# Optimization experiments

Hardware: AMD Instinct MI355X
Metric: run time of the kernel (lower is better)

Reference implementation:

```python
import jax, jax.numpy as jnp
import numpy as np

E = 1024   # embed_dim
H = 16     # num_heads
D = E // H # head_dim = 64
S = 8192   # cache length
LN_EPS = 1e-6  # flax LayerNorm default


def _ln(x, scale, bias):
    m = jnp.mean(x, axis=-1, keepdims=True)
    v = jnp.mean(jnp.square(x - m), axis=-1, keepdims=True)
    return (x - m) * jax.lax.rsqrt(v + LN_EPS) * scale + bias


def setup_inputs() -> dict:
    key = jax.random.key(0)
    ks = jax.random.split(key, 16)
    w = lambda k, shape: jax.random.normal(k, shape, jnp.float32) * 0.02
    return {
        "x": jax.random.normal(ks[0], (E,), jnp.float32),
        "cache": jax.random.normal(ks[1], (2, S, H, D), jnp.float32),
        "Wv": w(ks[2], (E, E)), "bv": jnp.zeros((E,), jnp.float32),
        "Wq": w(ks[3], (E, E)), "bq": jnp.zeros((E,), jnp.float32),
        "Wk": w(ks[4], (E, E)), "bk": jnp.zeros((E,), jnp.float32),
        "Wo": w(ks[5], (E, E)), "bo": jnp.zeros((E,), jnp.float32),
        "W1": w(ks[6], (E, E)), "b1": jnp.zeros((E,), jnp.float32),
        "W2": w(ks[7], (E, E)), "b2": jnp.zeros((E,), jnp.float32),
        "ln1_s": jnp.ones((E,), jnp.float32), "ln1_b": jnp.zeros((E,), jnp.float32),
        "ln2_s": jnp.ones((E,), jnp.float32), "ln2_b": jnp.zeros((E,), jnp.float32),
        "eval_flag": 1,
    }


def reference(x, cache, Wv, bv, Wq, bq, Wk, bk, Wo, bo,
              W1, b1, W2, b2, ln1_s, ln1_b, ln2_s, ln2_b, eval_flag):
    # --- attention with shifting KV cache ---
    v_i = (x @ Wv + bv).reshape(1, H, D)
    q_i = (x @ Wq + bq).reshape(H, D)
    k_i = (x @ Wk + bk).reshape(1, H, D)
    v = jnp.concatenate((cache[0, 1:], v_i), axis=0)  # [S, H, D]
    k = jnp.concatenate((cache[1, 1:], k_i), axis=0)  # [S, H, D]
    mask = jnp.any(v != 0, axis=(1, 2))               # [S]
    attn = jnp.einsum('hd,khd->hk', q_i, k) / jnp.sqrt(jnp.float32(D))
    attn = jnp.where(mask, attn, -jnp.inf)
    attn = jax.nn.softmax(attn, axis=-1)              # [H, S]
    values = jnp.einsum('hk,khd->hd', attn, v).reshape(E)
    out_i = values @ Wo + bo
    new_cache = jnp.stack([v, k])                     # [2, S, H, D]

    # --- residual + LN + FFN (dropout deterministic => identity) ---
    h = _ln(x + out_i, ln1_s, ln1_b)
    ff = jax.nn.relu(h @ W1 + b1) @ W2 + b2
    h = _ln(h + ff, ln2_s, ln2_b)
    return (h, new_cache)
```

## Files before the change

### kernel.cpp

```cpp
#include <hip/hip_runtime.h>
#include <hip/hip_bf16.h>

#define SLEN 8192
#define EDIM 1024
#define NB2  512

typedef float f4 __attribute__((ext_vector_type(4)));


__device__ inline float2 blockSum512_2(float2 v, float2* lds) {
#pragma unroll
    for (int off = 32; off; off >>= 1) {
        v.x += __shfl_xor(v.x, off);
        v.y += __shfl_xor(v.y, off);
    }
    int w = threadIdx.x >> 6, ln = threadIdx.x & 63;
    __syncthreads();
    if (ln == 0) lds[w] = v;
    __syncthreads();
    float2 s = {0.f, 0.f};
#pragma unroll
    for (int i = 0; i < 8; ++i) { s.x += lds[i].x; s.y += lds[i].y; }
    return s;
}

__device__ inline float2 blockSum1024_2(float2 v, float2* lds) {
#pragma unroll
    for (int off = 32; off; off >>= 1) {
        v.x += __shfl_xor(v.x, off);
        v.y += __shfl_xor(v.y, off);
    }
    int w = threadIdx.x >> 6, ln = threadIdx.x & 63;
    __syncthreads();
    if (ln == 0) lds[w] = v;
    __syncthreads();
    float2 s = {0.f, 0.f};
#pragma unroll
    for (int i = 0; i < 16; ++i) { s.x += lds[i].x; s.y += lds[i].y; }
    return s;
}

__global__ __launch_bounds__(256) void qkv_partial(
    const float* __restrict__ Wq, const float* __restrict__ Wk,
    const float* __restrict__ Wv, const float* __restrict__ x,
    float* __restrict__ part) {
    int cg_ = blockIdx.x;
    int m = cg_ >> 2;
    const float* W = (m == 0) ? Wq : ((m == 1) ? Wk : Wv);
    int col = (cg_ & 3) * 256 + threadIdx.x;
    int r0 = blockIdx.y * 64;
    float acc = 0.f;
#pragma unroll 16
    for (int r = 0; r < 64; ++r)
        acc = fmaf(x[r0 + r], W[(r0 + r) * EDIM + col], acc);
    part[((size_t)m * 16 + blockIdx.y) * EDIM + col] = acc;
}

__global__ __launch_bounds__(512) void attn_copy(
    const float* __restrict__ cache,
    const float* __restrict__ qkvp,
    const float* __restrict__ bq, const float* __restrict__ bk,
    const float* __restrict__ bv,
    float* __restrict__ nv, float* __restrict__ nk,
    float* __restrict__ flag, float* __restrict__ score) {
    __shared__ float qs_l[1024];
    __shared__ float aux[1024];
    int b = blockIdx.x, tid = threadIdx.x;
    int w = tid >> 6, ld = tid & 63;
    int c = b >> 1;
    bool isK = (b & 1) != 0;
    int s0 = c * 16 + w * 2;

    if (isK) {
#pragma unroll
        for (int j = 0; j < 2; ++j) {
            int i = tid + 512 * j;
            float v = bq[i];
#pragma unroll
            for (int sl = 0; sl < 16; ++sl) v += qkvp[sl * EDIM + i];
            qs_l[i] = v * 0.125f;
        }
        if (b == 1023) {
#pragma unroll
            for (int j = 0; j < 2; ++j) {
                int i = tid + 512 * j;
                float v = bk[i];
#pragma unroll
                for (int sl = 0; sl < 16; ++sl) v += qkvp[(16 + sl) * EDIM + i];
                aux[i] = v;
            }
        }
    } else if (b == 1022) {
#pragma unroll
        for (int j = 0; j < 2; ++j) {
            int i = tid + 512 * j;
            float v = bv[i];
#pragma unroll
            for (int sl = 0; sl < 16; ++sl) v += qkvp[(32 + sl) * EDIM + i];
            aux[i] = v;
        }
    }
    __syncthreads();

    if (!isK) {
        f4 vv[2][4];
#pragma unroll
        for (int p = 0; p < 2; ++p) {
            int s = s0 + p;
            const float* src = (s < SLEN - 1) ? cache + (size_t)(s + 1) * EDIM
                                              : aux;
#pragma unroll
            for (int it = 0; it < 4; ++it)
                vv[p][it] = *(const f4*)(src + it * 256 + ld * 4);
        }
#pragma unroll
        for (int p = 0; p < 2; ++p) {
            int s = s0 + p;
            unsigned nzb = 0u;
#pragma unroll
            for (int it = 0; it < 4; ++it) {
                *(f4*)(nv + (size_t)s * EDIM + it * 256 + ld * 4) = vv[p][it];
                nzb |= __float_as_uint(vv[p][it].x) | __float_as_uint(vv[p][it].y) |
                       __float_as_uint(vv[p][it].z) | __float_as_uint(vv[p][it].w);
            }
            bool anynz = (__ballot(nzb != 0u) != 0ull);
            if (ld == 0) flag[s] = anynz ? 1.f : 0.f;
        }
    } else {
        f4 q4[4];
#pragma unroll
        for (int it = 0; it < 4; ++it)
            q4[it] = *(const f4*)&qs_l[it * 256 + ld * 4];
        f4 kv[2][4];
#pragma unroll
        for (int p = 0; p < 2; ++p) {
            int s = s0 + p;
            const float* src = (s < SLEN - 1) ? cache + (size_t)(SLEN + s + 1) * EDIM
                                              : aux;
#pragma unroll
            for (int it = 0; it < 4; ++it)
                kv[p][it] = *(const f4*)(src + it * 256 + ld * 4);
        }
#pragma unroll
        for (int p = 0; p < 2; ++p) {
            int s = s0 + p;
#pragma unroll
            for (int it = 0; it < 4; ++it) {
                *(f4*)(nk + (size_t)s * EDIM + it * 256 + ld * 4) = kv[p][it];
                float d = q4[it].x * kv[p][it].x + q4[it].y * kv[p][it].y +
                          q4[it].z * kv[p][it].z + q4[it].w * kv[p][it].w;
                d += __shfl_xor(d, 1);
                d += __shfl_xor(d, 2);
                d += __shfl_xor(d, 4);
                d += __shfl_xor(d, 8);
                if ((ld & 15) == 0) score[s * 16 + it * 4 + (ld >> 4)] = d;
            }
        }
    }
}

__global__ __launch_bounds__(512) void attn_wv(
    const float* __restrict__ nv, const float* __restrict__ flag,
    const float* __restrict__ score,
    float* __restrict__ l2, float* __restrict__ acc2) {
    __shared__ float sw[8][16];
    __shared__ float sacc[8][16][64];
    int tid = threadIdx.x;
    int w = tid >> 6, ld = tid & 63;
    int s0 = blockIdx.x * 16 + w * 2;

    float wgsum[4];
    f4 acc[4];
#pragma unroll
    for (int it = 0; it < 4; ++it) {
        wgsum[it] = 0.f;
        acc[it] = (f4){0.f, 0.f, 0.f, 0.f};
    }
#pragma unroll
    for (int p = 0; p < 2; ++p) {
        int s = s0 + p;
        f4 vv[4];
#pragma unroll
        for (int it = 0; it < 4; ++it)
            vv[it] = *(const f4*)(nv + (size_t)s * EDIM + it * 256 + ld * 4);
        float fl = flag[s];
#pragma unroll
        for (int it = 0; it < 4; ++it) {
            int h = it * 4 + (ld >> 4);
            float wg = (fl != 0.f) ? __expf(score[s * 16 + h]) : 0.f;
            wgsum[it] += wg;
            acc[it].x = fmaf(wg, vv[it].x, acc[it].x);
            acc[it].y = fmaf(wg, vv[it].y, acc[it].y);
            acc[it].z = fmaf(wg, vv[it].z, acc[it].z);
            acc[it].w = fmaf(wg, vv[it].w, acc[it].w);
        }
    }
    if ((ld & 15) == 0) {
#pragma unroll
        for (int it = 0; it < 4; ++it) sw[w][it * 4 + (ld >> 4)] = wgsum[it];
    }
#pragma unroll
    for (int it = 0; it < 4; ++it) {
        int h = it * 4 + (ld >> 4);
        *(f4*)&sacc[w][h][(ld & 15) * 4] = acc[it];
    }
    __syncthreads();

#pragma unroll
    for (int j = 0; j < 2; ++j) {
        int h = 2 * w + j;
        float a = 0.f;
#pragma unroll
        for (int ww = 0; ww < 8; ++ww) a += sacc[ww][h][ld];
        acc2[(size_t)blockIdx.x * 1024 + h * 64 + ld] = a;
        if (ld == 0) {
            float l = 0.f;
#pragma unroll
            for (int ww = 0; ww < 8; ++ww) l += sw[ww][h];
            l2[blockIdx.x * 16 + h] = l;
        }
    }
}

__global__ __launch_bounds__(256) void attn_red(
    const float* __restrict__ l2, const float* __restrict__ acc2,
    float* __restrict__ l3g, float* __restrict__ acc3) {
    __shared__ float sA[4][64];
    __shared__ float sLl[4][16];
    int cx = blockIdx.x, g = blockIdx.y;
    int t = threadIdx.x, w = t >> 6, ld = t & 63;
    int p0 = g * 64 + w * 16;
    float a = 0.f;
#pragma unroll
    for (int i = 0; i < 16; ++i)
        a += acc2[(size_t)(p0 + i) * 1024 + cx * 64 + ld];
    sA[w][ld] = a;
    if (cx == 0 && ld < 16) {
        float l = 0.f;
#pragma unroll
        for (int i = 0; i < 16; ++i) l += l2[(p0 + i) * 16 + ld];
        sLl[w][ld] = l;
    }
    __syncthreads();
    if (w == 0) {
        acc3[(size_t)g * 1024 + cx * 64 + ld] =
            sA[0][ld] + sA[1][ld] + sA[2][ld] + sA[3][ld];
        if (cx == 0 && ld < 16)
            l3g[g * 16 + ld] = sLl[0][ld] + sLl[1][ld] + sLl[2][ld] + sLl[3][ld];
    }
}

__global__ __launch_bounds__(512) void gemv_wo(
    const float* __restrict__ Wo,
    const float* __restrict__ l3g, const float* __restrict__ acc3,
    float* __restrict__ part) {
    __shared__ float vals[64];
    __shared__ float sred[2][256];
    int by = blockIdx.y;
    int t = threadIdx.x;
    if (t < 64) {
        float a = 0.f, L = 0.f;
#pragma unroll
        for (int g = 0; g < 8; ++g) {
            a += acc3[(size_t)g * 1024 + by * 64 + t];
            L += l3g[g * 16 + by];
        }
        vals[t] = a / L;
    }
    __syncthreads();
    int half = t >> 8, tc = t & 255;
    int col = blockIdx.x * 256 + tc;
    float acc = 0.f;
#pragma unroll 16
    for (int r = 0; r < 32; ++r)
        acc = fmaf(vals[half * 32 + r],
                   Wo[(size_t)(by * 64 + half * 32 + r) * EDIM + col], acc);
    sred[half][tc] = acc;
    __syncthreads();
    if (t < 256)
        part[(size_t)by * EDIM + blockIdx.x * 256 + t] = sred[0][t] + sred[1][t];
}

__global__ __launch_bounds__(512) void gemv_w1(
    const float* __restrict__ W1, const float* __restrict__ gp1,
    const float* __restrict__ bo, const float* __restrict__ x,
    const float* __restrict__ ln1s, const float* __restrict__ ln1b,
    float* __restrict__ h1, float* __restrict__ part) {
    __shared__ float r_l[1024];
    __shared__ float2 red[8];
    __shared__ float vals[64];
    __shared__ float sred[2][256];
    int t = threadIdx.x;
    float2 ss = {0.f, 0.f};
#pragma unroll
    for (int j = 0; j < 2; ++j) {
        int i = t + 512 * j;
        float v = x[i] + bo[i];
#pragma unroll
        for (int sl = 0; sl < 16; ++sl) v += gp1[(size_t)sl * EDIM + i];
        r_l[i] = v;
        ss.x += v; ss.y += v * v;
    }
    float2 s = blockSum512_2(ss, red);
    float mean = s.x * (1.f / 1024.f);
    float var = s.y * (1.f / 1024.f) - mean * mean;
    float rstd = rsqrtf(var + 1e-6f);
    int by = blockIdx.y;
    if (t < 64) {
        int row = by * 64 + t;
        float hv = (r_l[row] - mean) * rstd * ln1s[row] + ln1b[row];
        vals[t] = hv;
        if (blockIdx.x == 0) h1[row] = hv;
    }
    __syncthreads();
    int half = t >> 8, tc = t & 255;
    int col = blockIdx.x * 256 + tc;
    float acc = 0.f;
#pragma unroll 16
    for (int r = 0; r < 32; ++r)
        acc = fmaf(vals[half * 32 + r],
                   W1[(size_t)(by * 64 + half * 32 + r) * EDIM + col], acc);
    sred[half][tc] = acc;
    __syncthreads();
    if (t < 256)
        part[(size_t)by * EDIM + blockIdx.x * 256 + t] = sred[0][t] + sred[1][t];
}

__global__ __launch_bounds__(512) void gemv_w2(
    const float* __restrict__ W2, const float* __restrict__ gp2,
    const float* __restrict__ b1, float* __restrict__ part) {
    __shared__ float vals[64];
    __shared__ float sred[2][256];
    int by = blockIdx.y;
    int t = threadIdx.x;
    if (t < 64) {
        int r = by * 64 + t;
        float v = b1[r];
#pragma unroll
        for (int sl = 0; sl < 16; ++sl) v += gp2[(size_t)sl * EDIM + r];
        vals[t] = fmaxf(v, 0.f);
    }
    __syncthreads();
    int half = t >> 8, tc = t & 255;
    int col = blockIdx.x * 256 + tc;
    float acc = 0.f;
#pragma unroll 16
    for (int r = 0; r < 32; ++r)
        acc = fmaf(vals[half * 32 + r],
                   W2[(size_t)(by * 64 + half * 32 + r) * EDIM + col], acc);
    sred[half][tc] = acc;
    __syncthreads();
    if (t < 256)
        part[(size_t)by * EDIM + blockIdx.x * 256 + t] = sred[0][t] + sred[1][t];
}

__global__ __launch_bounds__(1024) void combine_ln(
    const float* __restrict__ part, const float* __restrict__ bias,
    const float* __restrict__ resid, const float* __restrict__ g,
    const float* __restrict__ b, float* __restrict__ out) {
    __shared__ float2 lds[16];
    int t = threadIdx.x;
    float v = bias[t];
#pragma unroll
    for (int sl = 0; sl < 16; ++sl) v += part[(size_t)sl * EDIM + t];
    float r = resid[t] + v;
    float2 s = blockSum1024_2((float2){r, r * r}, lds);
    float mean = s.x * (1.f / 1024.f);
    float var = s.y * (1.f / 1024.f) - mean * mean;
    out[t] = (r - mean) * rsqrtf(var + 1e-6f) * g[t] + b[t];
}

extern "C" void kernel_launch(void* const* d_in, const int* in_sizes, int n_in,
                              void* d_out, int out_size, void* d_ws, size_t ws_size,
                              hipStream_t stream) {
    const float* x     = (const float*)d_in[0];
    const float* cache = (const float*)d_in[1];
    const float* Wv    = (const float*)d_in[2];
    const float* bv    = (const float*)d_in[3];
    const float* Wq    = (const float*)d_in[4];
    const float* bq    = (const float*)d_in[5];
    const float* Wk    = (const float*)d_in[6];
    const float* bk    = (const float*)d_in[7];
    const float* Wo    = (const float*)d_in[8];
    const float* bo    = (const float*)d_in[9];
    const float* W1    = (const float*)d_in[10];
    const float* b1    = (const float*)d_in[11];
    const float* W2    = (const float*)d_in[12];
    const float* b2    = (const float*)d_in[13];
    const float* ln1s  = (const float*)d_in[14];
    const float* ln1b  = (const float*)d_in[15];
    const float* ln2s  = (const float*)d_in[16];
    const float* ln2b  = (const float*)d_in[17];

    float* out = (float*)d_out;
    float* nv = out + 1024;
    float* nk = out + 1024 + (size_t)SLEN * EDIM;

    float* w     = (float*)d_ws;
    float* qkvp  = w;
    float* flag  = qkvp + 48 * 1024;
    float* score = flag + SLEN;
    float* l2    = score + (size_t)SLEN * 16;
    float* acc2  = l2 + (size_t)NB2 * 16;
    float* l3g   = acc2 + (size_t)NB2 * 1024;
    float* acc3  = l3g + 128;
    float* gp1   = acc3 + 8 * 1024;
    float* h1    = gp1 + 16 * 1024;
    float* gp2   = h1 + 1024;
    float* gp3   = gp2 + 16 * 1024;

    qkv_partial<<<dim3(12, 16), 256, 0, stream>>>(Wq, Wk, Wv, x, qkvp);
    attn_copy<<<1024, 512, 0, stream>>>(cache, qkvp, bq, bk, bv, nv, nk, flag, score);
    attn_wv<<<NB2, 512, 0, stream>>>(nv, flag, score, l2, acc2);
    attn_red<<<dim3(16, 8), 256, 0, stream>>>(l2, acc2, l3g, acc3);
    gemv_wo<<<dim3(4, 16), 512, 0, stream>>>(Wo, l3g, acc3, gp1);
    gemv_w1<<<dim3(4, 16), 512, 0, stream>>>(W1, gp1, bo, x, ln1s, ln1b, h1, gp2);
    gemv_w2<<<dim3(4, 16), 512, 0, stream>>>(W2, gp2, b1, gp3);
    combine_ln<<<1, 1024, 0, stream>>>(gp3, b2, h1, ln2s, ln2b, out);
}
```

Baseline: 56.67 us.

## Fuse V cache copy with weighted-value accumulation, split K copy kernel

The combined K/V copy kernel is split into a K kernel (copy plus QK scores) and a V kernel that copies the V cache and immediately uses the loaded values for the softmax-weighted accumulation. This removes the re-read of the new V cache (32 MB) from global memory and the flag buffer round trip. The mask is now computed in registers via a ballot. A barrier is added because the aux buffer now aliases the shared accumulation array.

```diff
diff --git a/kernel.cpp b/kernel.cpp
--- a/kernel.cpp
+++ b/kernel.cpp
@@ -56,41 +56,84 @@
     part[((size_t)m * 16 + blockIdx.y) * EDIM + col] = acc;
 }
 
-__global__ __launch_bounds__(512) void attn_copy(
+__global__ __launch_bounds__(512) void attn_copyK(
     const float* __restrict__ cache,
     const float* __restrict__ qkvp,
     const float* __restrict__ bq, const float* __restrict__ bk,
-    const float* __restrict__ bv,
-    float* __restrict__ nv, float* __restrict__ nk,
-    float* __restrict__ flag, float* __restrict__ score) {
+    float* __restrict__ nk, float* __restrict__ score) {
     __shared__ float qs_l[1024];
     __shared__ float aux[1024];
-    int b = blockIdx.x, tid = threadIdx.x;
+    int tid = threadIdx.x;
     int w = tid >> 6, ld = tid & 63;
-    int c = b >> 1;
-    bool isK = (b & 1) != 0;
-    int s0 = c * 16 + w * 2;
-
-    if (isK) {
+    int s0 = blockIdx.x * 16 + w * 2;
+
+#pragma unroll
+    for (int j = 0; j < 2; ++j) {
+        int i = tid + 512 * j;
+        float v = bq[i];
+#pragma unroll
+        for (int sl = 0; sl < 16; ++sl) v += qkvp[sl * EDIM + i];
+        qs_l[i] = v * 0.125f;
+    }
+    if (blockIdx.x == 511) {
 #pragma unroll
         for (int j = 0; j < 2; ++j) {
             int i = tid + 512 * j;
-            float v = bq[i];
-#pragma unroll
-            for (int sl = 0; sl < 16; ++sl) v += qkvp[sl * EDIM + i];
-            qs_l[i] = v * 0.125f;
-        }
-        if (b == 1023) {
-#pragma unroll
-            for (int j = 0; j < 2; ++j) {
-                int i = tid + 512 * j;
-                float v = bk[i];
-#pragma unroll
-                for (int sl = 0; sl < 16; ++sl) v += qkvp[(16 + sl) * EDIM + i];
-                aux[i] = v;
-            }
-        }
-    } else if (b == 1022) {
+            float v = bk[i];
+#pragma unroll
+            for (int sl = 0; sl < 16; ++sl) v += qkvp[(16 + sl) * EDIM + i];
+            aux[i] = v;
+        }
+    }
+    __syncthreads();
+
+    f4 q4[4];
+#pragma unroll
+    for (int it = 0; it < 4; ++it)
+        q4[it] = *(const f4*)&qs_l[it * 256 + ld * 4];
+
+    f4 kv[2][4];
+#pragma unroll
+    for (int p = 0; p < 2; ++p) {
+        int s = s0 + p;
+        const float* src = (s < SLEN - 1) ? cache + (size_t)(SLEN + s + 1) * EDIM
+                                          : aux;
+#pragma unroll
+        for (int it = 0; it < 4; ++it)
+            kv[p][it] = *(const f4*)(src + it * 256 + ld * 4);
+    }
+#pragma unroll
+    for (int p = 0; p < 2; ++p) {
+        int s = s0 + p;
+#pragma unroll
+        for (int it = 0; it < 4; ++it) {
+            *(f4*)(nk + (size_t)s * EDIM + it * 256 + ld * 4) = kv[p][it];
+            float d = q4[it].x * kv[p][it].x + q4[it].y * kv[p][it].y +
+                      q4[it].z * kv[p][it].z + q4[it].w * kv[p][it].w;
+            d += __shfl_xor(d, 1);
+            d += __shfl_xor(d, 2);
+            d += __shfl_xor(d, 4);
+            d += __shfl_xor(d, 8);
+            if ((ld & 15) == 0) score[s * 16 + it * 4 + (ld >> 4)] = d;
+        }
+    }
+}
+
+__global__ __launch_bounds__(512) void attn_copyV(
+    const float* __restrict__ cache,
+    const float* __restrict__ qkvp,
+    const float* __restrict__ bv,
+    const float* __restrict__ score,
+    float* __restrict__ nv,
+    float* __restrict__ l2, float* __restrict__ acc2) {
+    __shared__ float sw[8][16];
+    __shared__ float sacc[8][16][64];
+    float* aux = &sacc[0][0][0];
+    int tid = threadIdx.x;
+    int w = tid >> 6, ld = tid & 63;
+    int s0 = blockIdx.x * 16 + w * 2;
+
+    if (blockIdx.x == NB2 - 1) {
 #pragma unroll
         for (int j = 0; j < 2; ++j) {
             int i = tid + 512 * j;
@@ -102,72 +145,23 @@
     }
     __syncthreads();
 
-    if (!isK) {
-        f4 vv[2][4];
-#pragma unroll
-        for (int p = 0; p < 2; ++p) {
-            int s = s0 + p;
-            const float* src = (s < SLEN - 1) ? cache + (size_t)(s + 1) * EDIM
-                                              : aux;
-#pragma unroll
-            for (int it = 0; it < 4; ++it)
-                vv[p][it] = *(const f4*)(src + it * 256 + ld * 4);
-        }
-#pragma unroll
-        for (int p = 0; p < 2; ++p) {
-            int s = s0 + p;
-            unsigned nzb = 0u;
-#pragma unroll
-            for (int it = 0; it < 4; ++it) {
-                *(f4*)(nv + (size_t)s * EDIM + it * 256 + ld * 4) = vv[p][it];
-                nzb |= __float_as_uint(vv[p][it].x) | __float_as_uint(vv[p][it].y) |
-                       __float_as_uint(vv[p][it].z) | __float_as_uint(vv[p][it].w);
-            }
-            bool anynz = (__ballot(nzb != 0u) != 0ull);
-            if (ld == 0) flag[s] = anynz ? 1.f : 0.f;
-        }
-    } else {
-        f4 q4[4];
+    f4 vv[2][4];
+#pragma unroll
+    for (int p = 0; p < 2; ++p) {
+        int s = s0 + p;
+        const float* src = (s < SLEN - 1) ? cache + (size_t)(s + 1) * EDIM
+                                          : aux;
 #pragma unroll
         for (int it = 0; it < 4; ++it)
-            q4[it] = *(const f4*)&qs_l[it * 256 + ld * 4];
-        f4 kv[2][4];
-#pragma unroll
-        for (int p = 0; p < 2; ++p) {
-            int s = s0 + p;
-            const float* src = (s < SLEN - 1) ? cache + (size_t)(SLEN + s + 1) * EDIM
-                                              : aux;
-#pragma unroll
-            for (int it = 0; it < 4; ++it)
-                kv[p][it] = *(const f4*)(src + it * 256 + ld * 4);
-        }
-#pragma unroll
-        for (int p = 0; p < 2; ++p) {
-            int s = s0 + p;
-#pragma unroll
-            for (int it = 0; it < 4; ++it) {
-                *(f4*)(nk + (size_t)s * EDIM + it * 256 + ld * 4) = kv[p][it];
-                float d = q4[it].x * kv[p][it].x + q4[it].y * kv[p][it].y +
-                          q4[it].z * kv[p][it].z + q4[it].w * kv[p][it].w;
-                d += __shfl_xor(d, 1);
-                d += __shfl_xor(d, 2);
-                d += __shfl_xor(d, 4);
-                d += __shfl_xor(d, 8);
-                if ((ld & 15) == 0) score[s * 16 + it * 4 + (ld >> 4)] = d;
-            }
-        }
-    }
-}
-
-__global__ __launch_bounds__(512) void attn_wv(
-    const float* __restrict__ nv, const float* __restrict__ flag,
-    const float* __restrict__ score,
-    float* __restrict__ l2, float* __restrict__ acc2) {
-    __shared__ float sw[8][16];
-    __shared__ float sacc[8][16][64];
-    int tid = threadIdx.x;
-    int w = tid >> 6, ld = tid & 63;
-    int s0 = blockIdx.x * 16 + w * 2;
+            vv[p][it] = *(const f4*)(src + it * 256 + ld * 4);
+    }
+#pragma unroll
+    for (int p = 0; p < 2; ++p) {
+        int s = s0 + p;
+#pragma unroll
+        for (int it = 0; it < 4; ++it)
+            *(f4*)(nv + (size_t)s * EDIM + it * 256 + ld * 4) = vv[p][it];
+    }
 
     float wgsum[4];
     f4 acc[4];
@@ -179,26 +173,29 @@
 #pragma unroll
     for (int p = 0; p < 2; ++p) {
         int s = s0 + p;
-        f4 vv[4];
+        unsigned nzb = 0u;
 #pragma unroll
         for (int it = 0; it < 4; ++it)
-            vv[it] = *(const f4*)(nv + (size_t)s * EDIM + it * 256 + ld * 4);
-        float fl = flag[s];
+            nzb |= __float_as_uint(vv[p][it].x) | __float_as_uint(vv[p][it].y) |
+                   __float_as_uint(vv[p][it].z) | __float_as_uint(vv[p][it].w);
+        bool allz = (__ballot(nzb != 0u) == 0ull);
 #pragma unroll
         for (int it = 0; it < 4; ++it) {
             int h = it * 4 + (ld >> 4);
-            float wg = (fl != 0.f) ? __expf(score[s * 16 + h]) : 0.f;
+            float wg = allz ? 0.f : __expf(score[s * 16 + h]);
             wgsum[it] += wg;
-            acc[it].x = fmaf(wg, vv[it].x, acc[it].x);
-            acc[it].y = fmaf(wg, vv[it].y, acc[it].y);
-            acc[it].z = fmaf(wg, vv[it].z, acc[it].z);
-            acc[it].w = fmaf(wg, vv[it].w, acc[it].w);
+            acc[it].x = fmaf(wg, vv[p][it].x, acc[it].x);
+            acc[it].y = fmaf(wg, vv[p][it].y, acc[it].y);
+            acc[it].z = fmaf(wg, vv[p][it].z, acc[it].z);
+            acc[it].w = fmaf(wg, vv[p][it].w, acc[it].w);
         }
     }
     if ((ld & 15) == 0) {
 #pragma unroll
         for (int it = 0; it < 4; ++it) sw[w][it * 4 + (ld >> 4)] = wgsum[it];
     }
+    __syncthreads();
+
 #pragma unroll
     for (int it = 0; it < 4; ++it) {
         int h = it * 4 + (ld >> 4);
@@ -398,8 +395,7 @@
 
     float* w     = (float*)d_ws;
     float* qkvp  = w;
-    float* flag  = qkvp + 48 * 1024;
-    float* score = flag + SLEN;
+    float* score = qkvp + 48 * 1024;
     float* l2    = score + (size_t)SLEN * 16;
     float* acc2  = l2 + (size_t)NB2 * 16;
     float* l3g   = acc2 + (size_t)NB2 * 1024;
@@ -410,8 +406,8 @@
     float* gp3   = gp2 + 16 * 1024;
 
     qkv_partial<<<dim3(12, 16), 256, 0, stream>>>(Wq, Wk, Wv, x, qkvp);
-    attn_copy<<<1024, 512, 0, stream>>>(cache, qkvp, bq, bk, bv, nv, nk, flag, score);
-    attn_wv<<<NB2, 512, 0, stream>>>(nv, flag, score, l2, acc2);
+    attn_copyK<<<512, 512, 0, stream>>>(cache, qkvp, bq, bk, nk, score);
+    attn_copyV<<<NB2, 512, 0, stream>>>(cache, qkvp, bv, score, nv, l2, acc2);
     attn_red<<<dim3(16, 8), 256, 0, stream>>>(l2, acc2, l3g, acc3);
     gemv_wo<<<dim3(4, 16), 512, 0, stream>>>(Wo, l3g, acc3, gp1);
     gemv_w1<<<dim3(4, 16), 512, 0, stream>>>(W1, gp1, bo, x, ln1s, ln1b, h1, gp2);
```

New measurement: 52.07 us. -8.1%, faster.
